# Kernel optimization log

Hardware: AMD Instinct MI355X
Metric: run time of the kernel (lower is better)

## Reference

```python
import jax, jax.numpy as jnp
import numpy as np

N_EMBD = 512
BLOCK = 512
HEADS = 16
HEAD_DIM = N_EMBD // HEADS
EPS = 1e-5


def _layernorm(x, g, b):
    mu = jnp.mean(x, axis=-1, keepdims=True)
    var = jnp.mean(jnp.square(x - mu), axis=-1, keepdims=True)
    return (x - mu) * jax.lax.rsqrt(var + EPS) * g + b


def setup_inputs() -> dict:
    key = jax.random.key(0)
    ks = jax.random.split(key, 12)
    B, T, C, H, D = 64, BLOCK, N_EMBD, HEADS, HEAD_DIM
    s = lambda fan_in: 1.0 / np.sqrt(fan_in)
    return {
        "x": jax.random.normal(ks[0], (B, T, C), dtype=jnp.float32),
        # per-head projections, stored (H, C, D) so y = einsum('btc,hcd->bhtd')
        "Wq": jax.random.normal(ks[1], (H, C, D), dtype=jnp.float32) * s(C),
        "Wk": jax.random.normal(ks[2], (H, C, D), dtype=jnp.float32) * s(C),
        "Wv": jax.random.normal(ks[3], (H, C, D), dtype=jnp.float32) * s(C),
        "Wp": jax.random.normal(ks[4], (C, C), dtype=jnp.float32) * s(C),
        "bp": jnp.zeros((C,), dtype=jnp.float32),
        "W1": jax.random.normal(ks[5], (C, 4 * C), dtype=jnp.float32) * s(C),
        "b1": jnp.zeros((4 * C,), dtype=jnp.float32),
        "W2": jax.random.normal(ks[6], (4 * C, C), dtype=jnp.float32) * s(4 * C),
        "b2": jnp.zeros((C,), dtype=jnp.float32),
        "g_ln1": jnp.ones((C,), dtype=jnp.float32),
        "b_ln1": jnp.zeros((C,), dtype=jnp.float32),
        "g_ln2": jnp.ones((C,), dtype=jnp.float32),
        "b_ln2": jnp.zeros((C,), dtype=jnp.float32),
    }


def reference(x, Wq, Wk, Wv, Wp, bp, W1, b1, W2, b2, g_ln1, b_ln1, g_ln2, b_ln2):
    B, T, C = x.shape
    h = _layernorm(x, g_ln1, b_ln1)
    q = jnp.einsum('btc,hcd->bhtd', h, Wq)
    k = jnp.einsum('btc,hcd->bhtd', h, Wk)
    v = jnp.einsum('btc,hcd->bhtd', h, Wv)
    wei = jnp.einsum('bhtd,bhsd->bhts', q, k) * (HEAD_DIM ** -0.5)
    causal = jnp.tril(jnp.ones((T, T), dtype=bool))
    wei = jnp.where(causal, wei, -jnp.inf)
    wei = jax.nn.softmax(wei, axis=-1)  # dropout = identity (eval mode)
    out = jnp.einsum('bhts,bhsd->bhtd', wei, v)
    out = out.transpose(0, 2, 1, 3).reshape(B, T, C)  # concat heads
    sa = out @ Wp + bp
    x = x + sa
    h2 = _layernorm(x, g_ln2, b_ln2)
    ff = jax.nn.relu(h2 @ W1 + b1) @ W2 + b2
    return x + ff
```

## Files before the change

### kernel.cpp

```cpp
#include <hip/hip_runtime.h>
#include <stdint.h>


typedef __attribute__((ext_vector_type(8))) short bf16x8;
typedef __attribute__((ext_vector_type(4))) short bf16x4;
typedef __attribute__((ext_vector_type(4))) float f32x4;

__device__ __forceinline__ unsigned short f2bf(float x) {
  union { float f; unsigned u; } v; v.f = x;
  unsigned r = v.u + 0x7fff + ((v.u >> 16) & 1);
  return (unsigned short)(r >> 16);
}

#if __has_builtin(__builtin_amdgcn_exp2f)
__device__ __forceinline__ float exp2fast(float x) { return __builtin_amdgcn_exp2f(x); }
#else
__device__ __forceinline__ float exp2fast(float x) { return exp2f(x); }
#endif

__device__ __forceinline__ unsigned cvtpk(float lo, float hi) {
  unsigned r; asm("v_cvt_pk_bf16_f32 %0, %1, %2" : "=v"(r) : "v"(lo), "v"(hi)); return r;
}

__device__ __forceinline__ f32x4 MFMA32(bf16x8 a, bf16x8 b, f32x4 c) {
  return __builtin_amdgcn_mfma_f32_16x16x32_bf16(a, b, c, 0, 0, 0);
}

#if __has_builtin(__builtin_amdgcn_mfma_f32_16x16x16bf16_1k)
__device__ __forceinline__ f32x4 MFMA16(bf16x4 a, bf16x4 b, f32x4 c) {
  return __builtin_amdgcn_mfma_f32_16x16x16bf16_1k(a, b, c, 0, 0, 0);
}
#else
__device__ __forceinline__ f32x4 MFMA16(bf16x4 a, bf16x4 b, f32x4 c) {
  f32x4 d;
  asm volatile("v_mfma_f32_16x16x16_bf16 %0, %1, %2, %3\n\ts_nop 7\n\ts_nop 3"
               : "=v"(d) : "v"(a), "v"(b), "v"(c));
  return d;
}
#endif

__device__ __forceinline__ void gload_lds16(const void* g, void* l) {
  __builtin_amdgcn_global_load_lds(
      (const __attribute__((address_space(1))) unsigned int*)(uintptr_t)g,
      (__attribute__((address_space(3))) unsigned int*)(unsigned)(uintptr_t)l,
      16, 0, 0);
}

#define WAITV8() do { asm volatile("s_waitcnt vmcnt(8)" ::: "memory"); } while (0)
#define WAITV0() do { asm volatile("s_waitcnt vmcnt(0)" ::: "memory"); } while (0)
#define WAITL0() do { asm volatile("s_waitcnt lgkmcnt(0)" ::: "memory"); } while (0)
#define SBAR()   __builtin_amdgcn_s_barrier()
#define SCHED0() __builtin_amdgcn_sched_barrier(0)

__global__ __launch_bounds__(256) void prep_qkv_w(
    const float* __restrict__ Wq, const float* __restrict__ Wk,
    const float* __restrict__ Wv, unsigned short* __restrict__ dst)
{
  __shared__ float tile[64 * 33];
  const int b = blockIdx.x;
  const int q = b / 128, hh = (b >> 3) & 15, kt = (b & 7) << 6;
  const float* W = (q == 0) ? Wq : ((q == 1) ? Wk : Wv);
  const int t = threadIdx.x;
  const int rr = t >> 2, ch = (t & 3) << 3;
  const float* sp = W + ((size_t)hh * 512 + kt + rr) * 32 + ch;
  float4 v0 = *(const float4*)(sp), v1 = *(const float4*)(sp + 4);
  float* dp = &tile[rr * 33 + ch];
  dp[0] = v0.x; dp[1] = v0.y; dp[2] = v0.z; dp[3] = v0.w;
  dp[4] = v1.x; dp[5] = v1.y; dp[6] = v1.z; dp[7] = v1.w;
  __syncthreads();
  const int d = t >> 3, toct = (t & 7) << 3;
  bf16x8 o;
#pragma unroll
  for (int j = 0; j < 8; ++j) o[j] = (short)f2bf(tile[(toct + j) * 33 + d]);
  *(bf16x8*)(dst + ((size_t)q * 512 + hh * 32 + d) * 512 + kt + toct) = o;
}

__global__ __launch_bounds__(256) void transpose_cast(
    const float* __restrict__ src, unsigned short* __restrict__ dst, int Kd, int Nd)
{
  __shared__ float tile[64 * 65];
  const int nk = Kd >> 6;
  const int kt = (blockIdx.x % nk) << 6, nt = (blockIdx.x / nk) << 6;
  const int t = threadIdx.x;
  const int rr = t >> 2, ch = (t & 3) << 4;
  const float* sp = src + (size_t)(kt + rr) * Nd + nt + ch;
  float* dp = &tile[rr * 65 + ch];
#pragma unroll
  for (int c = 0; c < 4; ++c) {
    float4 v = *(const float4*)(sp + c * 4);
    dp[c * 4 + 0] = v.x; dp[c * 4 + 1] = v.y; dp[c * 4 + 2] = v.z; dp[c * 4 + 3] = v.w;
  }
  __syncthreads();
  const int nn = t >> 2, c2 = (t & 3) << 4;
  bf16x8 o0, o1;
#pragma unroll
  for (int j = 0; j < 8; ++j) {
    o0[j] = (short)f2bf(tile[(c2 + j) * 65 + nn]);
    o1[j] = (short)f2bf(tile[(c2 + 8 + j) * 65 + nn]);
  }
  unsigned short* op = dst + (size_t)(nt + nn) * Kd + kt + c2;
  *(bf16x8*)(op) = o0;
  *(bf16x8*)(op + 8) = o1;
}

__global__ __launch_bounds__(256) void ln_kernel(
    const float* __restrict__ x, const float* __restrict__ g,
    const float* __restrict__ b, unsigned short* __restrict__ out)
{
  const int lane = threadIdx.x & 63;
  const size_t row = (size_t)blockIdx.x * 4 + (threadIdx.x >> 6);
  const float* xp = x + row * 512 + lane * 8;
  float xv[8] __attribute__((aligned(16)));
  *(float4*)(xv)     = *(const float4*)(xp);
  *(float4*)(xv + 4) = *(const float4*)(xp + 4);
  float s = 0.f, s2 = 0.f;
#pragma unroll
  for (int j = 0; j < 8; ++j) { s += xv[j]; s2 += xv[j] * xv[j]; }
#pragma unroll
  for (int m = 1; m < 64; m <<= 1) { s += __shfl_xor(s, m); s2 += __shfl_xor(s2, m); }
  float mean = s * (1.f / 512.f);
  float rstd = rsqrtf(fmaxf(s2 * (1.f / 512.f) - mean * mean, 0.f) + 1e-5f);
  float gv[8] __attribute__((aligned(16))), bv[8] __attribute__((aligned(16)));
  *(float4*)(gv)     = *(const float4*)(g + lane * 8);
  *(float4*)(gv + 4) = *(const float4*)(g + lane * 8 + 4);
  *(float4*)(bv)     = *(const float4*)(b + lane * 8);
  *(float4*)(bv + 4) = *(const float4*)(b + lane * 8 + 4);
  bf16x8 o;
#pragma unroll
  for (int j = 0; j < 8; ++j) o[j] = (short)f2bf((xv[j] - mean) * rstd * gv[j] + bv[j]);
  *(bf16x8*)(out + row * 512 + lane * 8) = o;
}

__global__ __launch_bounds__(256) void vt_kernel(
    const unsigned short* __restrict__ vnat, unsigned short* __restrict__ vt)
{
  __shared__ unsigned short tile[64 * 36];
  const int bh = blockIdx.x >> 3, tt = (blockIdx.x & 7) << 6;
  const int tid = threadIdx.x;
  const int rr = tid >> 2, ch = tid & 3;
  bf16x8 v = *(const bf16x8*)(vnat + ((size_t)bh * 512 + tt + rr) * 32 + ch * 8);
  unsigned short* dst = &tile[rr * 36 + ch * 8];
#pragma unroll
  for (int j = 0; j < 8; ++j) dst[j] = (unsigned short)v[j];
  __syncthreads();
  const int d = tid >> 3, toct = (tid & 7) << 3;
  union { unsigned short s[8]; bf16x8 v8; } o;
#pragma unroll
  for (int j = 0; j < 8; ++j) o.s[j] = tile[(toct + j) * 36 + d];
  *(bf16x8*)(vt + ((size_t)bh * 32 + d) * 512 + tt + toct) = o.v8;
}

template <int MODE, int P, int KT, int NBY>
__device__ __forceinline__ void gemm_persist(
    const unsigned short* __restrict__ A, const unsigned short* __restrict__ Bt,
    int N,
    unsigned short* __restrict__ obf, float* __restrict__ of32,
    const float* __restrict__ bias, const float* __restrict__ resid,
    unsigned short* __restrict__ vout)
{
  constexpr int K = KT * 64;
  constexpr int TOT = P * KT;
  __shared__ __align__(16) unsigned short As[2][256 * 64];
  __shared__ __align__(16) unsigned short Bs[2][256 * 64];
  const int tid = threadIdx.x, lane = tid & 63, wid = tid >> 6;
  const int wr = wid >> 2, wc = wid & 3;
  const int r = lane & 15, hq = lane >> 4;

  const int tau0 = (blockIdx.x & 7) * (32 * P) + (blockIdx.x >> 3) * P;

  const int srow = wid * 32 + (lane >> 3);
  const int schunk = ((lane & 7) ^ ((lane >> 3) & 7)) * 8;

  auto STAGE_A = [&](int g2) {
    const int m2 = g2 / KT, kt2 = g2 % KT;
    const int bx = (tau0 + m2) / NBY;
    const unsigned short* src = A + (size_t)(bx * 256 + srow) * K + kt2 * 64 + schunk;
    char* dst = (char*)(&As[g2 & 1][0]) + wid * 4096;
#pragma unroll
    for (int g = 0; g < 4; ++g) gload_lds16(src + (size_t)g * 8 * K, dst + g * 1024);
  };
  auto STAGE_B = [&](int g2) {
    const int m2 = g2 / KT, kt2 = g2 % KT;
    const int tau = tau0 + m2;
    const int by = tau - (tau / NBY) * NBY;
    const unsigned short* src = Bt + (size_t)(by * 256 + srow) * K + kt2 * 64 + schunk;
    char* dst = (char*)(&Bs[g2 & 1][0]) + wid * 4096;
#pragma unroll
    for (int g = 0; g < 4; ++g) gload_lds16(src + (size_t)g * 8 * K, dst + g * 1024);
  };

  const int x0 = ((hq) ^ (r & 7)) * 16;
  const int x1 = ((4 + hq) ^ (r & 7)) * 16;
  const int abase = (wr * 128 + r) * 128;
  const int bbase = (wc * 64 + r) * 128;

  f32x4 acc[8][4] = {};
  bf16x8 af[4][2], bfa[2][2], bfb[2][2];

  STAGE_A(0); STAGE_B(0);
  STAGE_A(1); STAGE_B(1);
  WAITV8(); SCHED0();
  SBAR();

#pragma unroll 1
  for (int p = 0; p < P; ++p) {
#pragma unroll 2
    for (int t = 0; t < KT; ++t) {
      const int g = p * KT + t;
      const int g2 = g + 2;
      const char* Ab = (const char*)(&As[g & 1][0]);
      const char* Bb = (const char*)(&Bs[g & 1][0]);
#pragma unroll
      for (int m = 0; m < 4; ++m) {
        af[m][0] = *(const bf16x8*)(Ab + abase + m * 2048 + x0);
        af[m][1] = *(const bf16x8*)(Ab + abase + m * 2048 + x1);
      }
#pragma unroll
      for (int n = 0; n < 2; ++n) {
        bfa[n][0] = *(const bf16x8*)(Bb + bbase + n * 2048 + x0);
        bfa[n][1] = *(const bf16x8*)(Bb + bbase + n * 2048 + x1);
      }
      WAITL0(); SCHED0();
      __builtin_amdgcn_s_setprio(1);
#pragma unroll
      for (int m = 0; m < 4; ++m)
#pragma unroll
        for (int n = 0; n < 2; ++n) {
          acc[m][n] = MFMA32(af[m][0], bfa[n][0], acc[m][n]);
          acc[m][n] = MFMA32(af[m][1], bfa[n][1], acc[m][n]);
        }
      __builtin_amdgcn_s_setprio(0);
      SBAR();
#pragma unroll
      for (int n = 0; n < 2; ++n) {
        bfb[n][0] = *(const bf16x8*)(Bb + bbase + (n + 2) * 2048 + x0);
        bfb[n][1] = *(const bf16x8*)(Bb + bbase + (n + 2) * 2048 + x1);
      }
      WAITL0(); SCHED0();
      __builtin_amdgcn_s_setprio(1);
#pragma unroll
      for (int m = 0; m < 4; ++m)
#pragma unroll
        for (int n = 0; n < 2; ++n) {
          acc[m][n + 2] = MFMA32(af[m][0], bfb[n][0], acc[m][n + 2]);
          acc[m][n + 2] = MFMA32(af[m][1], bfb[n][1], acc[m][n + 2]);
        }
      __builtin_amdgcn_s_setprio(0);
      SBAR();
#pragma unroll
      for (int m = 0; m < 4; ++m) {
        af[m][0] = *(const bf16x8*)(Ab + abase + 8192 + m * 2048 + x0);
        af[m][1] = *(const bf16x8*)(Ab + abase + 8192 + m * 2048 + x1);
      }
      if (g2 < TOT) STAGE_B(g2);
      WAITL0(); SCHED0();
      __builtin_amdgcn_s_setprio(1);
#pragma unroll
      for (int m = 0; m < 4; ++m)
#pragma unroll
        for (int n = 0; n < 2; ++n) {
          acc[4 + m][n] = MFMA32(af[m][0], bfa[n][0], acc[4 + m][n]);
          acc[4 + m][n] = MFMA32(af[m][1], bfa[n][1], acc[4 + m][n]);
        }
      __builtin_amdgcn_s_setprio(0);
      SBAR();
      if (g2 < TOT) STAGE_A(g2);
      __builtin_amdgcn_s_setprio(1);
#pragma unroll
      for (int m = 0; m < 4; ++m)
#pragma unroll
        for (int n = 0; n < 2; ++n) {
          acc[4 + m][n + 2] = MFMA32(af[m][0], bfb[n][0], acc[4 + m][n + 2]);
          acc[4 + m][n + 2] = MFMA32(af[m][1], bfb[n][1], acc[4 + m][n + 2]);
        }
      __builtin_amdgcn_s_setprio(0);
      if (g2 < TOT) { WAITV8(); } else { WAITV0(); }
      SCHED0();
      SBAR();
    }

    {
      const int tau = tau0 + p;
      const int bx = tau / NBY, by = tau - bx * NBY;
      const int brow = bx << 8, bcol = by << 8;
#pragma unroll
      for (int m = 0; m < 8; ++m)
#pragma unroll
        for (int n = 0; n < 4; ++n) {
          const int row0 = brow + wr * 128 + m * 16 + hq * 4;
          const int col = bcol + wc * 64 + n * 16 + r;
#pragma unroll
          for (int q2 = 0; q2 < 4; ++q2) {
            const int row = row0 + q2;
            float v = acc[m][n][q2];
            if (MODE == 1) {
              const int which = col >> 9, hh = (col >> 5) & 15, dd = col & 31;
              const int bb = row >> 9, tt = row & 511;
              const size_t off = ((((size_t)bb) * 16 + hh) * 512 + tt) * 32 + dd;
              if (which < 2) {
                if (which == 0) v *= 0.25503521f;
                obf[(size_t)which * 16777216 + off] = f2bf(v);
              } else
                vout[off] = f2bf(v);
            } else if (MODE == 2) {
              v += bias[col] + resid[(size_t)row * N + col];
              of32[(size_t)row * N + col] = v;
            } else if (MODE == 3) {
              v = fmaxf(v + bias[col], 0.f);
              obf[(size_t)row * N + col] = f2bf(v);
            }
            acc[m][n][q2] = 0.f;
          }
        }
    }
  }
}

__global__ __launch_bounds__(512, 2) void qkv_gemm(
    const unsigned short* __restrict__ A, const unsigned short* __restrict__ Bt,
    unsigned short* __restrict__ obf, unsigned short* __restrict__ vout)
{ gemm_persist<1, 3, 8, 6>(A, Bt, 1536, obf, nullptr, nullptr, nullptr, vout); }

__global__ __launch_bounds__(512, 2) void proj_gemm(
    const unsigned short* __restrict__ A, const unsigned short* __restrict__ Bt,
    float* __restrict__ of32, const float* __restrict__ bias,
    const float* __restrict__ resid)
{ gemm_persist<2, 1, 8, 2>(A, Bt, 512, nullptr, of32, bias, resid, nullptr); }

__global__ __launch_bounds__(512, 2) void ffn1_gemm(
    const unsigned short* __restrict__ A, const unsigned short* __restrict__ Bt,
    unsigned short* __restrict__ obf, const float* __restrict__ bias)
{ gemm_persist<3, 4, 8, 8>(A, Bt, 2048, obf, nullptr, bias, nullptr, nullptr); }

__global__ __launch_bounds__(512, 2) void ffn2_gemm(
    const unsigned short* __restrict__ A, const unsigned short* __restrict__ Bt,
    float* __restrict__ of32, const float* __restrict__ bias,
    const float* __restrict__ resid)
{ gemm_persist<2, 1, 32, 2>(A, Bt, 512, nullptr, of32, bias, resid, nullptr); }

__global__ __launch_bounds__(512, 4) void attn_kernel(
    const unsigned short* __restrict__ Qb, const unsigned short* __restrict__ Kb,
    const unsigned short* __restrict__ Vt, unsigned short* __restrict__ att)
{
  __shared__ __align__(16) unsigned short Ks[512 * 32];
  __shared__ __align__(16) unsigned short Vs[32 * 512];
  const int tid = threadIdx.x, lane = tid & 63, wid = tid >> 6;
  const int bh = blockIdx.x;
  const int r = lane & 15, hq = lane >> 4;
  const unsigned short* Kg = Kb + (size_t)bh * (512 * 32);
  const unsigned short* Vg = Vt + (size_t)bh * (32 * 512);
#pragma unroll
  for (int it = 0; it < 4; ++it) {
    const int c = it * 512 + tid;
    gload_lds16(Kg + c * 8, (char*)Ks + (it * 512 + wid * 64) * 16);
    const int d = c >> 6, sb = c & 63;
    gload_lds16(Vg + d * 512 + (sb ^ (d & 15)) * 8, (char*)Vs + (it * 512 + wid * 64) * 16);
  }
  __syncthreads();

  const f32x4 z = {0.f, 0.f, 0.f, 0.f};
  for (int p = 0; p < 4; ++p) {
    const int t0 = (((p >> 1) << 4) + ((p & 1) ? 15 - wid : wid)) << 4;
    const bf16x8 qf = *(const bf16x8*)(Qb + ((size_t)bh * 512 + t0 + r) * 32 + hq * 8);
    f32x4 o0 = z, o1 = z;
    float m = -1e30f, l = 0.f;
    const int s0m = t0 & ~31;
    for (int s0 = 0; s0 <= s0m; s0 += 32) {
      f32x4 st0 = MFMA32(*(const bf16x8*)((const char*)Ks + (s0 + r) * 64 + hq * 16), qf, z);
      f32x4 st1 = MFMA32(*(const bf16x8*)((const char*)Ks + (s0 + 16 + r) * 64 + hq * 16), qf, z);
      if (s0 == s0m) {
        const int qq = t0 + r;
#pragma unroll
        for (int j = 0; j < 4; ++j) {
          if (s0 + 4 * hq + j > qq)      st0[j] = -1e30f;
          if (s0 + 16 + 4 * hq + j > qq) st1[j] = -1e30f;
        }
      }
      float mx = fmaxf(fmaxf(fmaxf(st0[0], st0[1]), fmaxf(st0[2], st0[3])),
                       fmaxf(fmaxf(st1[0], st1[1]), fmaxf(st1[2], st1[3])));
      mx = fmaxf(mx, __shfl_xor(mx, 16));
      mx = fmaxf(mx, __shfl_xor(mx, 32));
      if (!__all(mx <= m + 8.f)) {
        const float mn = fmaxf(m, mx);
        const float f = exp2fast(m - mn);
        m = mn; l *= f; o0 *= f; o1 *= f;
      }
      float p0[4], p1[4];
#pragma unroll
      for (int j = 0; j < 4; ++j) {
        p0[j] = exp2fast(st0[j] - m);
        p1[j] = exp2fast(st1[j] - m);
      }
      float rs = ((p0[0] + p0[1]) + (p0[2] + p0[3])) + ((p1[0] + p1[1]) + (p1[2] + p1[3]));
      rs += __shfl_xor(rs, 16);
      rs += __shfl_xor(rs, 32);
      l += rs;
      union { unsigned u[2]; bf16x4 v; } a0, a1;
      a0.u[0] = cvtpk(p0[0], p0[1]); a0.u[1] = cvtpk(p0[2], p0[3]);
      a1.u[0] = cvtpk(p1[0], p1[1]); a1.u[1] = cvtpk(p1[2], p1[3]);
      const int lb = (s0 >> 3) + (hq >> 1);
      const char* vb = (const char*)Vs + (hq & 1) * 8;
      o0 = MFMA16(a0.v, *(const bf16x4*)(vb + r * 1024 + ((lb) ^ r) * 16), o0);
      o0 = MFMA16(a1.v, *(const bf16x4*)(vb + r * 1024 + ((lb + 2) ^ r) * 16), o0);
      o1 = MFMA16(a0.v, *(const bf16x4*)(vb + (r + 16) * 1024 + ((lb) ^ r) * 16), o1);
      o1 = MFMA16(a1.v, *(const bf16x4*)(vb + (r + 16) * 1024 + ((lb + 2) ^ r) * 16), o1);
    }
    const size_t ob = ((size_t)(bh >> 4) * 512) * 512 + (size_t)((bh & 15) * 32);
#pragma unroll
    for (int j = 0; j < 4; ++j) {
      const float li = 1.f / __shfl(l, 4 * hq + j);
      const size_t rowb = ob + (size_t)(t0 + 4 * hq + j) * 512;
      att[rowb + r]      = f2bf(o0[j] * li);
      att[rowb + 16 + r] = f2bf(o1[j] * li);
    }
  }
}

extern "C" void kernel_launch(void* const* d_in, const int* in_sizes, int n_in,
                              void* d_out, int out_size, void* d_ws, size_t ws_size,
                              hipStream_t stream)
{
  const float* x   = (const float*)d_in[0];
  const float* Wq  = (const float*)d_in[1];
  const float* Wk  = (const float*)d_in[2];
  const float* Wv  = (const float*)d_in[3];
  const float* Wp  = (const float*)d_in[4];
  const float* bp  = (const float*)d_in[5];
  const float* W1  = (const float*)d_in[6];
  const float* b1  = (const float*)d_in[7];
  const float* W2  = (const float*)d_in[8];
  const float* b2  = (const float*)d_in[9];
  const float* g1  = (const float*)d_in[10];
  const float* bb1 = (const float*)d_in[11];
  const float* g2  = (const float*)d_in[12];
  const float* bb2 = (const float*)d_in[13];
  float* out = (float*)d_out;

  char* ws = (char*)d_ws;
  unsigned short* h    = (unsigned short*)(ws);
  unsigned short* wqkv = (unsigned short*)(ws + 33554432);
  unsigned short* wp   = (unsigned short*)(ws + 35127296);
  unsigned short* w1   = (unsigned short*)(ws + 35651584);
  unsigned short* w2   = (unsigned short*)(ws + 37748736);
  unsigned short* qk   = (unsigned short*)(ws + 39845888);
  unsigned short* vt   = qk + (size_t)2 * 16777216;
  unsigned short* att  = vt + 16777216;
  unsigned short* vnat = att;
  unsigned short* mid  = qk;
  if (ws_size < 174063616) return;

  prep_qkv_w<<<384, 256, 0, stream>>>(Wq, Wk, Wv, wqkv);
  transpose_cast<<<64, 256, 0, stream>>>(Wp, wp, 512, 512);
  transpose_cast<<<256, 256, 0, stream>>>(W1, w1, 512, 2048);
  transpose_cast<<<256, 256, 0, stream>>>(W2, w2, 2048, 512);

  ln_kernel<<<8192, 256, 0, stream>>>(x, g1, bb1, h);

  qkv_gemm<<<256, 512, 0, stream>>>(h, wqkv, qk, vnat);

  vt_kernel<<<8192, 256, 0, stream>>>(vnat, vt);

  attn_kernel<<<1024, 512, 0, stream>>>(qk, qk + 16777216, vt, att);

  proj_gemm<<<256, 512, 0, stream>>>(att, wp, out, bp, x);

  ln_kernel<<<8192, 256, 0, stream>>>(out, g2, bb2, h);

  ffn1_gemm<<<256, 512, 0, stream>>>(h, w1, mid, b1);

  ffn2_gemm<<<256, 512, 0, stream>>>(mid, w2, out, b2, out);
}
```

Before: 387.3 us.

## Software-pipeline LDS fragment loads across k-steps with partial lgkmcnt waits

Restructures the GEMM inner loop so the next k-step's A/B fragments are read from LDS during the last MFMA block of the current step. Partial lgkmcnt waits let MFMAs start before all outstanding LDS reads finish. The number of barriers per iteration drops from four to two. This adds an extra register array for the second A half, which raises register pressure, and it reorders the global-to-LDS staging against the barriers.

```diff
diff --git a/kernel.cpp b/kernel.cpp
--- a/kernel.cpp
+++ b/kernel.cpp
@@ -48,9 +48,11 @@
 
 #define WAITV8() do { asm volatile("s_waitcnt vmcnt(8)" ::: "memory"); } while (0)
 #define WAITV0() do { asm volatile("s_waitcnt vmcnt(0)" ::: "memory"); } while (0)
-#define WAITL0() do { asm volatile("s_waitcnt lgkmcnt(0)" ::: "memory"); } while (0)
+#define WAITL(N) do { asm volatile("s_waitcnt lgkmcnt(" #N ")" ::: "memory"); } while (0)
 #define SBAR()   __builtin_amdgcn_s_barrier()
 #define SCHED0() __builtin_amdgcn_sched_barrier(0)
+#define PRIO1()  __builtin_amdgcn_s_setprio(1)
+#define PRIO0()  __builtin_amdgcn_s_setprio(0)
 
 __global__ __launch_bounds__(256) void prep_qkv_w(
     const float* __restrict__ Wq, const float* __restrict__ Wk,
@@ -195,12 +197,27 @@
   const int bbase = (wc * 64 + r) * 128;
 
   f32x4 acc[8][4] = {};
-  bf16x8 af[4][2], bfa[2][2], bfb[2][2];
+  bf16x8 af[4][2], ag[4][2], bfa[2][2], bfb[2][2];
+
+  auto LOAD_ENTRY = [&](const char* Ab, const char* Bb) {
+#pragma unroll
+    for (int m2 = 0; m2 < 4; ++m2) {
+      af[m2][0] = *(const bf16x8*)(Ab + abase + m2 * 2048 + x0);
+      af[m2][1] = *(const bf16x8*)(Ab + abase + m2 * 2048 + x1);
+    }
+#pragma unroll
+    for (int n2 = 0; n2 < 2; ++n2) {
+      bfa[n2][0] = *(const bf16x8*)(Bb + bbase + n2 * 2048 + x0);
+      bfa[n2][1] = *(const bf16x8*)(Bb + bbase + n2 * 2048 + x1);
+    }
+  };
 
   STAGE_A(0); STAGE_B(0);
   STAGE_A(1); STAGE_B(1);
   WAITV8(); SCHED0();
   SBAR();
+  LOAD_ENTRY((const char*)(&As[0][0]), (const char*)(&Bs[0][0]));
+  SCHED0();
 
 #pragma unroll 1
   for (int p = 0; p < P; ++p) {
@@ -210,18 +227,16 @@
       const int g2 = g + 2;
       const char* Ab = (const char*)(&As[g & 1][0]);
       const char* Bb = (const char*)(&Bs[g & 1][0]);
-#pragma unroll
-      for (int m = 0; m < 4; ++m) {
-        af[m][0] = *(const bf16x8*)(Ab + abase + m * 2048 + x0);
-        af[m][1] = *(const bf16x8*)(Ab + abase + m * 2048 + x1);
-      }
-#pragma unroll
-      for (int n = 0; n < 2; ++n) {
-        bfa[n][0] = *(const bf16x8*)(Bb + bbase + n * 2048 + x0);
-        bfa[n][1] = *(const bf16x8*)(Bb + bbase + n * 2048 + x1);
-      }
-      WAITL0(); SCHED0();
-      __builtin_amdgcn_s_setprio(1);
+      const char* An = (const char*)(&As[(g + 1) & 1][0]);
+      const char* Bn = (const char*)(&Bs[(g + 1) & 1][0]);
+#pragma unroll
+      for (int n2 = 0; n2 < 2; ++n2) {
+        bfb[n2][0] = *(const bf16x8*)(Bb + bbase + (n2 + 2) * 2048 + x0);
+        bfb[n2][1] = *(const bf16x8*)(Bb + bbase + (n2 + 2) * 2048 + x1);
+      }
+      SCHED0();
+      WAITL(4); SCHED0();
+      PRIO1();
 #pragma unroll
       for (int m = 0; m < 4; ++m)
 #pragma unroll
@@ -229,15 +244,15 @@
           acc[m][n] = MFMA32(af[m][0], bfa[n][0], acc[m][n]);
           acc[m][n] = MFMA32(af[m][1], bfa[n][1], acc[m][n]);
         }
-      __builtin_amdgcn_s_setprio(0);
-      SBAR();
-#pragma unroll
-      for (int n = 0; n < 2; ++n) {
-        bfb[n][0] = *(const bf16x8*)(Bb + bbase + (n + 2) * 2048 + x0);
-        bfb[n][1] = *(const bf16x8*)(Bb + bbase + (n + 2) * 2048 + x1);
-      }
-      WAITL0(); SCHED0();
-      __builtin_amdgcn_s_setprio(1);
+      PRIO0();
+#pragma unroll
+      for (int m2 = 0; m2 < 4; ++m2) {
+        ag[m2][0] = *(const bf16x8*)(Ab + abase + 8192 + m2 * 2048 + x0);
+        ag[m2][1] = *(const bf16x8*)(Ab + abase + 8192 + m2 * 2048 + x1);
+      }
+      SCHED0();
+      WAITL(8); SCHED0();
+      PRIO1();
 #pragma unroll
       for (int m = 0; m < 4; ++m)
 #pragma unroll
@@ -245,38 +260,39 @@
           acc[m][n + 2] = MFMA32(af[m][0], bfb[n][0], acc[m][n + 2]);
           acc[m][n + 2] = MFMA32(af[m][1], bfb[n][1], acc[m][n + 2]);
         }
-      __builtin_amdgcn_s_setprio(0);
+      PRIO0();
+      WAITL(0); SCHED0();
+      PRIO1();
+#pragma unroll
+      for (int m = 0; m < 4; ++m)
+#pragma unroll
+        for (int n = 0; n < 2; ++n) {
+          acc[4 + m][n] = MFMA32(ag[m][0], bfa[n][0], acc[4 + m][n]);
+          acc[4 + m][n] = MFMA32(ag[m][1], bfa[n][1], acc[4 + m][n]);
+        }
+      PRIO0();
       SBAR();
-#pragma unroll
-      for (int m = 0; m < 4; ++m) {
-        af[m][0] = *(const bf16x8*)(Ab + abase + 8192 + m * 2048 + x0);
-        af[m][1] = *(const bf16x8*)(Ab + abase + 8192 + m * 2048 + x1);
-      }
-      if (g2 < TOT) STAGE_B(g2);
-      WAITL0(); SCHED0();
-      __builtin_amdgcn_s_setprio(1);
-#pragma unroll
-      for (int m = 0; m < 4; ++m)
-#pragma unroll
-        for (int n = 0; n < 2; ++n) {
-          acc[4 + m][n] = MFMA32(af[m][0], bfa[n][0], acc[4 + m][n]);
-          acc[4 + m][n] = MFMA32(af[m][1], bfa[n][1], acc[4 + m][n]);
-        }
-      __builtin_amdgcn_s_setprio(0);
-      SBAR();
-      if (g2 < TOT) STAGE_A(g2);
-      __builtin_amdgcn_s_setprio(1);
-#pragma unroll
-      for (int m = 0; m < 4; ++m)
-#pragma unroll
-        for (int n = 0; n < 2; ++n) {
-          acc[4 + m][n + 2] = MFMA32(af[m][0], bfb[n][0], acc[4 + m][n + 2]);
-          acc[4 + m][n + 2] = MFMA32(af[m][1], bfb[n][1], acc[4 + m][n + 2]);
-        }
-      __builtin_amdgcn_s_setprio(0);
-      if (g2 < TOT) { WAITV8(); } else { WAITV0(); }
+      if (g2 < TOT) {
+        STAGE_B(g2); STAGE_A(g2);
+        WAITV8();
+      } else {
+        WAITV0();
+      }
       SCHED0();
       SBAR();
+      if (g + 1 < TOT) {
+        LOAD_ENTRY(An, Bn);
+        SCHED0();
+      }
+      PRIO1();
+#pragma unroll
+      for (int m = 0; m < 4; ++m)
+#pragma unroll
+        for (int n = 0; n < 2; ++n) {
+          acc[4 + m][n + 2] = MFMA32(ag[m][0], bfb[n][0], acc[4 + m][n + 2]);
+          acc[4 + m][n + 2] = MFMA32(ag[m][1], bfb[n][1], acc[4 + m][n + 2]);
+        }
+      PRIO0();
     }
 
     {
```

Measured after the change: 409.0 us. 5.6% more time.

## Split global-to-LDS staging across warp phases and adjust prefetch distance

Applied to the files above, without the earlier changes.

The GEMM main loop now spreads the A and B tile staging loads across different compute phases by warp group. Half the waves issue their A loads at the top of the step and the other half after the first barrier, and B loads are split the same way across the third and fourth phases. A is prefetched one step ahead (g+1) instead of two, while B stays two steps ahead, and the vmcnt wait is changed to match. The aim is to spread the vector-memory issue pressure so it overlaps better with the MFMA phases. The shorter A prefetch distance and the changed wait counts could expose latency or create hazards on the double-buffered LDS if the counts are wrong.

```diff
diff --git a/kernel.cpp b/kernel.cpp
--- a/kernel.cpp
+++ b/kernel.cpp
@@ -46,11 +46,13 @@
       16, 0, 0);
 }
 
-#define WAITV8() do { asm volatile("s_waitcnt vmcnt(8)" ::: "memory"); } while (0)
+#define WAITVN(N) do { asm volatile("s_waitcnt vmcnt(" #N ")" ::: "memory"); } while (0)
 #define WAITV0() do { asm volatile("s_waitcnt vmcnt(0)" ::: "memory"); } while (0)
-#define WAITL0() do { asm volatile("s_waitcnt lgkmcnt(0)" ::: "memory"); } while (0)
+#define WAITL(N) do { asm volatile("s_waitcnt lgkmcnt(" #N ")" ::: "memory"); } while (0)
 #define SBAR()   __builtin_amdgcn_s_barrier()
 #define SCHED0() __builtin_amdgcn_sched_barrier(0)
+#define PRIO1()  __builtin_amdgcn_s_setprio(1)
+#define PRIO0()  __builtin_amdgcn_s_setprio(0)
 
 __global__ __launch_bounds__(256) void prep_qkv_w(
     const float* __restrict__ Wq, const float* __restrict__ Wk,
@@ -196,10 +198,12 @@
 
   f32x4 acc[8][4] = {};
   bf16x8 af[4][2], bfa[2][2], bfb[2][2];
+  const bool aPh1 = ((wid & 2) == 0);
+  const bool bPh3 = ((wid & 1) == 0);
 
   STAGE_A(0); STAGE_B(0);
   STAGE_A(1); STAGE_B(1);
-  WAITV8(); SCHED0();
+  WAITV0(); SCHED0();
   SBAR();
 
 #pragma unroll 1
@@ -207,9 +211,11 @@
 #pragma unroll 2
     for (int t = 0; t < KT; ++t) {
       const int g = p * KT + t;
-      const int g2 = g + 2;
       const char* Ab = (const char*)(&As[g & 1][0]);
       const char* Bb = (const char*)(&Bs[g & 1][0]);
+      const bool stA = (g >= 1) && (g + 1 < TOT);
+      const bool stB = (g + 2 < TOT);
+      if (stA && aPh1) STAGE_A(g + 1);
 #pragma unroll
       for (int m = 0; m < 4; ++m) {
         af[m][0] = *(const bf16x8*)(Ab + abase + m * 2048 + x0);
@@ -220,8 +226,8 @@
         bfa[n][0] = *(const bf16x8*)(Bb + bbase + n * 2048 + x0);
         bfa[n][1] = *(const bf16x8*)(Bb + bbase + n * 2048 + x1);
       }
-      WAITL0(); SCHED0();
-      __builtin_amdgcn_s_setprio(1);
+      WAITL(0); SCHED0();
+      PRIO1();
 #pragma unroll
       for (int m = 0; m < 4; ++m)
 #pragma unroll
@@ -229,15 +235,16 @@
           acc[m][n] = MFMA32(af[m][0], bfa[n][0], acc[m][n]);
           acc[m][n] = MFMA32(af[m][1], bfa[n][1], acc[m][n]);
         }
-      __builtin_amdgcn_s_setprio(0);
+      PRIO0();
       SBAR();
+      if (stA && !aPh1) STAGE_A(g + 1);
 #pragma unroll
       for (int n = 0; n < 2; ++n) {
         bfb[n][0] = *(const bf16x8*)(Bb + bbase + (n + 2) * 2048 + x0);
         bfb[n][1] = *(const bf16x8*)(Bb + bbase + (n + 2) * 2048 + x1);
       }
-      WAITL0(); SCHED0();
-      __builtin_amdgcn_s_setprio(1);
+      WAITL(0); SCHED0();
+      PRIO1();
 #pragma unroll
       for (int m = 0; m < 4; ++m)
 #pragma unroll
@@ -245,16 +252,16 @@
           acc[m][n + 2] = MFMA32(af[m][0], bfb[n][0], acc[m][n + 2]);
           acc[m][n + 2] = MFMA32(af[m][1], bfb[n][1], acc[m][n + 2]);
         }
-      __builtin_amdgcn_s_setprio(0);
+      PRIO0();
       SBAR();
+      if (stB && bPh3) STAGE_B(g + 2);
 #pragma unroll
       for (int m = 0; m < 4; ++m) {
         af[m][0] = *(const bf16x8*)(Ab + abase + 8192 + m * 2048 + x0);
         af[m][1] = *(const bf16x8*)(Ab + abase + 8192 + m * 2048 + x1);
       }
-      if (g2 < TOT) STAGE_B(g2);
-      WAITL0(); SCHED0();
-      __builtin_amdgcn_s_setprio(1);
+      WAITL(0); SCHED0();
+      PRIO1();
 #pragma unroll
       for (int m = 0; m < 4; ++m)
 #pragma unroll
@@ -262,10 +269,10 @@
           acc[4 + m][n] = MFMA32(af[m][0], bfa[n][0], acc[4 + m][n]);
           acc[4 + m][n] = MFMA32(af[m][1], bfa[n][1], acc[4 + m][n]);
         }
-      __builtin_amdgcn_s_setprio(0);
+      PRIO0();
       SBAR();
-      if (g2 < TOT) STAGE_A(g2);
-      __builtin_amdgcn_s_setprio(1);
+      if (stB && !bPh3) STAGE_B(g + 2);
+      PRIO1();
 #pragma unroll
       for (int m = 0; m < 4; ++m)
 #pragma unroll
@@ -273,8 +280,8 @@
           acc[4 + m][n + 2] = MFMA32(af[m][0], bfb[n][0], acc[4 + m][n + 2]);
           acc[4 + m][n + 2] = MFMA32(af[m][1], bfb[n][1], acc[4 + m][n + 2]);
         }
-      __builtin_amdgcn_s_setprio(0);
-      if (g2 < TOT) { WAITV8(); } else { WAITV0(); }
+      PRIO0();
+      if (stB) { WAITVN(4); } else { WAITV0(); }
       SCHED0();
       SBAR();
     }
```

New measurement: 384.3 us. Within noise of the previous version (-0.8%).

## Simplify GEMM main loop to single-stage prefetch with full-tile compute

Applied to the files above, without the earlier changes.

Replaces the hand-scheduled four-phase GEMM inner loop with a simpler one. The old loop interleaved LDS fragment loads, MFMA groups, s_setprio and several barriers, and kept two global-to-LDS stages in flight. The new loop issues the next tile's global-to-LDS copy at the top of each iteration, loads all B fragments and streams the A fragments through 32 MFMAs per k-step, then drains all outstanding loads and hits a single barrier. This cuts barrier count and leaves instruction scheduling to the compiler, but it reduces prefetch depth from two tiles to one and gives up explicit overlap of LDS reads with MFMA.

```diff
diff --git a/kernel.cpp b/kernel.cpp
--- a/kernel.cpp
+++ b/kernel.cpp
@@ -46,9 +46,7 @@
       16, 0, 0);
 }
 
-#define WAITV8() do { asm volatile("s_waitcnt vmcnt(8)" ::: "memory"); } while (0)
 #define WAITV0() do { asm volatile("s_waitcnt vmcnt(0)" ::: "memory"); } while (0)
-#define WAITL0() do { asm volatile("s_waitcnt lgkmcnt(0)" ::: "memory"); } while (0)
 #define SBAR()   __builtin_amdgcn_s_barrier()
 #define SCHED0() __builtin_amdgcn_sched_barrier(0)
 
@@ -195,11 +193,9 @@
   const int bbase = (wc * 64 + r) * 128;
 
   f32x4 acc[8][4] = {};
-  bf16x8 af[4][2], bfa[2][2], bfb[2][2];
 
   STAGE_A(0); STAGE_B(0);
-  STAGE_A(1); STAGE_B(1);
-  WAITV8(); SCHED0();
+  WAITV0(); SCHED0();
   SBAR();
 
 #pragma unroll 1
@@ -207,75 +203,26 @@
 #pragma unroll 2
     for (int t = 0; t < KT; ++t) {
       const int g = p * KT + t;
-      const int g2 = g + 2;
+      if (g + 1 < TOT) { STAGE_A(g + 1); STAGE_B(g + 1); }
       const char* Ab = (const char*)(&As[g & 1][0]);
       const char* Bb = (const char*)(&Bs[g & 1][0]);
-#pragma unroll
-      for (int m = 0; m < 4; ++m) {
-        af[m][0] = *(const bf16x8*)(Ab + abase + m * 2048 + x0);
-        af[m][1] = *(const bf16x8*)(Ab + abase + m * 2048 + x1);
+      bf16x8 bf[4][2];
+#pragma unroll
+      for (int n = 0; n < 4; ++n) {
+        bf[n][0] = *(const bf16x8*)(Bb + bbase + n * 2048 + x0);
+        bf[n][1] = *(const bf16x8*)(Bb + bbase + n * 2048 + x1);
       }
 #pragma unroll
-      for (int n = 0; n < 2; ++n) {
-        bfa[n][0] = *(const bf16x8*)(Bb + bbase + n * 2048 + x0);
-        bfa[n][1] = *(const bf16x8*)(Bb + bbase + n * 2048 + x1);
+      for (int m = 0; m < 8; ++m) {
+        const bf16x8 a0 = *(const bf16x8*)(Ab + abase + m * 2048 + x0);
+        const bf16x8 a1 = *(const bf16x8*)(Ab + abase + m * 2048 + x1);
+#pragma unroll
+        for (int n = 0; n < 4; ++n) {
+          acc[m][n] = MFMA32(a0, bf[n][0], acc[m][n]);
+          acc[m][n] = MFMA32(a1, bf[n][1], acc[m][n]);
+        }
       }
-      WAITL0(); SCHED0();
-      __builtin_amdgcn_s_setprio(1);
-#pragma unroll
-      for (int m = 0; m < 4; ++m)
-#pragma unroll
-        for (int n = 0; n < 2; ++n) {
-          acc[m][n] = MFMA32(af[m][0], bfa[n][0], acc[m][n]);
-          acc[m][n] = MFMA32(af[m][1], bfa[n][1], acc[m][n]);
-        }
-      __builtin_amdgcn_s_setprio(0);
-      SBAR();
-#pragma unroll
-      for (int n = 0; n < 2; ++n) {
-        bfb[n][0] = *(const bf16x8*)(Bb + bbase + (n + 2) * 2048 + x0);
-        bfb[n][1] = *(const bf16x8*)(Bb + bbase + (n + 2) * 2048 + x1);
-      }
-      WAITL0(); SCHED0();
-      __builtin_amdgcn_s_setprio(1);
-#pragma unroll
-      for (int m = 0; m < 4; ++m)
-#pragma unroll
-        for (int n = 0; n < 2; ++n) {
-          acc[m][n + 2] = MFMA32(af[m][0], bfb[n][0], acc[m][n + 2]);
-          acc[m][n + 2] = MFMA32(af[m][1], bfb[n][1], acc[m][n + 2]);
-        }
-      __builtin_amdgcn_s_setprio(0);
-      SBAR();
-#pragma unroll
-      for (int m = 0; m < 4; ++m) {
-        af[m][0] = *(const bf16x8*)(Ab + abase + 8192 + m * 2048 + x0);
-        af[m][1] = *(const bf16x8*)(Ab + abase + 8192 + m * 2048 + x1);
-      }
-      if (g2 < TOT) STAGE_B(g2);
-      WAITL0(); SCHED0();
-      __builtin_amdgcn_s_setprio(1);
-#pragma unroll
-      for (int m = 0; m < 4; ++m)
-#pragma unroll
-        for (int n = 0; n < 2; ++n) {
-          acc[4 + m][n] = MFMA32(af[m][0], bfa[n][0], acc[4 + m][n]);
-          acc[4 + m][n] = MFMA32(af[m][1], bfa[n][1], acc[4 + m][n]);
-        }
-      __builtin_amdgcn_s_setprio(0);
-      SBAR();
-      if (g2 < TOT) STAGE_A(g2);
-      __builtin_amdgcn_s_setprio(1);
-#pragma unroll
-      for (int m = 0; m < 4; ++m)
-#pragma unroll
-        for (int n = 0; n < 2; ++n) {
-          acc[4 + m][n + 2] = MFMA32(af[m][0], bfb[n][0], acc[4 + m][n + 2]);
-          acc[4 + m][n + 2] = MFMA32(af[m][1], bfb[n][1], acc[4 + m][n + 2]);
-        }
-      __builtin_amdgcn_s_setprio(0);
-      if (g2 < TOT) { WAITV8(); } else { WAITV0(); }
-      SCHED0();
+      WAITV0(); SCHED0();
       SBAR();
     }
 
```

After: 408.5 us. 1.05x slower.
